# Kernel optimization log

Measured on AMD Instinct MI355X. Metric: run time of the kernel, lower is better.

The kernel has to match this reference:

```python
import jax, jax.numpy as jnp
import numpy as np

HEAD = 2

def conv1x1(w, x):
    # 1x1 Conv1d, bias=False: (O,C) x (B,C,N) -> (B,O,N)
    return jnp.einsum('oc,bcn->bon', w, x)

def setup_inputs() -> dict:
    key = jax.random.key(0)
    ks = jax.random.split(key, 14)
    B, Cin, N = 8, 64, 50000
    L, K = 256, 32
    tc, Cout = 128, 128
    def w(k, o, c):
        return jax.random.normal(k, (o, c), jnp.float32) * (1.0 / np.sqrt(c))
    return {
        'in_feature': jax.random.normal(ks[0], (B, Cin, N), jnp.float32),
        'in_tokens': jax.random.normal(ks[1], (B, tc, L), jnp.float32),
        'knn_idx': jax.random.randint(ks[2], (B, L, K), 0, N),
        # dynamic_f: conv1x1(Cin->tc), ReLU, conv1x1(tc->tc)  (norm = Identity)
        'w_dyn1': w(ks[3], tc, Cin),
        'w_dyn2': w(ks[4], tc, tc),
        # feature_block: conv1x1(Cin->Cout) since input_dims != output_dims
        'w_fb': w(ks[5], Cout, Cin),
        # Transformer (token self-attention + FFN)
        'w_k': w(ks[6], tc // 2, tc),
        'w_q': w(ks[7], tc // 2, tc),
        'w_v': w(ks[8], tc, tc),
        'w_ff1': w(ks[9], 2 * tc, tc),
        'w_ff2': w(ks[10], tc, 2 * tc),
        # Projector (tokens -> points cross-attention)
        'w_pv': w(ks[11], Cout, tc),
        'w_pk': w(ks[12], Cout, tc),
        'w_pq': w(ks[13], Cout, Cout),
    }

def reference(in_feature, in_tokens, w_dyn1, w_dyn2, w_fb,
              w_k, w_q, w_v, w_ff1, w_ff2, w_pv, w_pk, w_pq, knn_idx):
    B, C, N = in_feature.shape
    _, L, K = knn_idx.shape
    h = HEAD

    # ---- KNN gather + max-pool over K neighbors -> (B, C, L) ----
    idx = knn_idx.reshape(B, 1, L * K)                      # broadcast over C
    gathered = jnp.take_along_axis(in_feature, idx, axis=2).reshape(B, C, L, K)
    pooled = gathered.max(axis=3)                           # (B, C, L)

    # ---- dynamic_f: conv1x1 -> ReLU -> conv1x1 ----
    tokens = conv1x1(w_dyn2, jax.nn.relu(conv1x1(w_dyn1, pooled)))  # (B, tc, L)
    tokens = tokens + in_tokens

    # ---- Transformer over tokens ----
    tc = tokens.shape[1]
    k = conv1x1(w_k, tokens).reshape(B, h, -1, L)
    q = conv1x1(w_q, tokens).reshape(B, h, -1, L)
    v = conv1x1(w_v, tokens).reshape(B, h, -1, L)
    kq = jnp.einsum('bhdn,bhdm->bhnm', k, q)                # (B, h, L, L)
    attn = jax.nn.softmax(kq / np.sqrt(kq.shape[2]), axis=2)
    kqv = jnp.einsum('bhdn,bhnm->bhdm', v, attn).reshape(B, tc, L)
    t = tokens + kqv
    t = t + conv1x1(w_ff2, jax.nn.relu(conv1x1(w_ff1, t)))  # (B, tc, L)

    # ---- feature_block (input_dims != output_dims) ----
    x = conv1x1(w_fb, in_feature)                           # (B, Cout, N)
    d = x.shape[1]

    # ---- Projector: tokens -> per-point features ----
    pv = conv1x1(w_pv, t).reshape(B, h, -1, L)
    pk = conv1x1(w_pk, t).reshape(B, h, -1, L)
    pq = conv1x1(w_pq, x).reshape(B, h, -1, N)
    coef = jax.nn.softmax(
        jnp.einsum('bhdl,bhdn->bhln', pk, pq) / np.sqrt(d / h), axis=2)  # softmax over tokens
    out_feature = x + jnp.einsum('bhdl,bhln->bhdn', pv, coef).reshape(B, d, N)
    return out_feature, t
```

## Files before the change

### kernel.cpp

```cpp
#include <hip/hip_runtime.h>

#define B 8
#define CIN 64
#define NPT 50000
#define L 256
#define TC 128

typedef unsigned short ushort_t;
typedef __bf16 bf16x8 __attribute__((ext_vector_type(8)));
typedef float f32x4 __attribute__((ext_vector_type(4)));

__device__ __forceinline__ ushort_t f2b(float v) {
    union { float f; unsigned int u; } x; x.f = v;
    unsigned int r = x.u + 0x7FFFu + ((x.u >> 16) & 1u);
    return (ushort_t)(r >> 16);
}

__global__ void k_gather(const float* __restrict__ f, const int* __restrict__ knn,
                         float* __restrict__ pooled) {
    int id = blockIdx.x * 256 + threadIdx.x;
    int l = id & 255;
    int c = (id >> 8) & 63;
    int b = id >> 14;
    const int* kn = knn + (b * L + l) * 32;
    const float* fr = f + (b * CIN + c) * NPT;
    float m = -1e30f;
    #pragma unroll 8
    for (int k = 0; k < 32; k++) m = fmaxf(m, fr[kn[k]]);
    pooled[(b * CIN + c) * L + l] = m;
}

template <int O, int C, bool RELU>
__global__ void k_conv(const float* __restrict__ in, const float* __restrict__ w,
                       const float* __restrict__ res, float* __restrict__ out,
                       float* __restrict__ out2, ushort_t* __restrict__ outb) {
    int id = blockIdx.x * 256 + threadIdx.x;
    int l = id & 255;
    int o = (id >> 8) % O;
    int b = id / (O * 256);
    const float* ir = in + b * C * L + l;
    const float* wr = w + o * C;
    float acc = 0.f;
    #pragma unroll 8
    for (int c = 0; c < C; c++) acc += wr[c] * ir[c * L];
    if (RELU) acc = fmaxf(acc, 0.f);
    if (res) acc += res[id];
    if (out)  out[id] = acc;
    if (out2) out2[id] = acc;
    if (outb) outb[id] = f2b(acc);
}

__global__ void k_attn(const float* __restrict__ kmat, const float* __restrict__ qmat,
                       float* __restrict__ attn) {
    int blk = blockIdx.x;
    int m = blk & 255;
    int h = (blk >> 8) & 1;
    int b = blk >> 9;
    int n = threadIdx.x;
    const float* kr = kmat + (b * 64 + h * 32) * L + n;
    const float* qr = qmat + (b * 64 + h * 32) * L + m;
    float s = 0.f;
    #pragma unroll
    for (int d = 0; d < 32; d++) s += kr[d * L] * qr[d * L];
    s *= (1.f / 16.f);
    __shared__ float sm[256];
    sm[n] = s;
    __syncthreads();
    for (int st = 128; st > 0; st >>= 1) { if (n < st) sm[n] = fmaxf(sm[n], sm[n + st]); __syncthreads(); }
    float mx = sm[0];
    __syncthreads();
    float p = __expf(s - mx);
    sm[n] = p;
    __syncthreads();
    for (int st = 128; st > 0; st >>= 1) { if (n < st) sm[n] += sm[n + st]; __syncthreads(); }
    float Z = sm[0];
    attn[((b * 2 + h) * L + n) * L + m] = p / Z;
}

__global__ void k_kqv(const float* __restrict__ vmat, const float* __restrict__ attn,
                      const float* __restrict__ tokens, float* __restrict__ t1) {
    int id = blockIdx.x * 256 + threadIdx.x;
    int m = id & 255;
    int ch = (id >> 8) & 127;
    int b = id >> 15;
    int h = ch >> 6;
    const float* vr = vmat + (b * TC + ch) * L;
    const float* ar = attn + ((b * 2 + h) * L) * L + m;
    float acc = 0.f;
    #pragma unroll 8
    for (int n = 0; n < L; n++) acc += vr[n] * ar[n * L];
    t1[id] = tokens[id] + acc;
}

__global__ void k_pkq(const float* __restrict__ pk, const float* __restrict__ wpq,
                      ushort_t* __restrict__ pkqo) {
    int id = blockIdx.x * 256 + threadIdx.x;
    int e = id & 127;
    int l = (id >> 7) & 255;
    int h = (id >> 15) & 1;
    int b = id >> 16;
    const float* pkr = pk + (b * TC + h * 64) * L + l;
    const float* wr = wpq + (h * 64) * TC + e;
    float acc = 0.f;
    #pragma unroll 8
    for (int d = 0; d < 64; d++) acc += pkr[d * L] * wr[d * TC];
    pkqo[id] = f2b(acc * 0.125f);
}

__global__ void k_cvt_w(const float* __restrict__ w, ushort_t* __restrict__ o, int n) {
    int i = blockIdx.x * 256 + threadIdx.x;
    if (i < n) o[i] = f2b(w[i]);
}

__global__ __launch_bounds__(256) void k_proj(const float* __restrict__ f,
                                              const ushort_t* __restrict__ wfb16,
                                              const ushort_t* __restrict__ pkq16,
                                              const ushort_t* __restrict__ pv16,
                                              float* __restrict__ out, int N) {
    const int b = blockIdx.y;
    const int n0 = blockIdx.x * 64;
    const int tid = threadIdx.x;
    const int w = tid >> 6;
    const int lane = tid & 63;
    const int g = lane >> 4, cc = lane & 15;
    const int p = w * 16 + cc;

    __shared__ __align__(16) ushort_t Pl[4][4096];
    __shared__ __align__(16) ushort_t xt[64 * 128];
    ushort_t* ft = &Pl[0][0];

    #pragma unroll
    for (int i = 0; i < 16; i++) {
        int lin = tid + i * 256;
        int c = lin >> 6, pp = lin & 63;
        int n = n0 + pp;
        float v = (n < N) ? f[((size_t)b * CIN + c) * N + n] : 0.f;
        int idx = pp * 64 + ((((c >> 3) ^ (pp & 7)) << 3)) + (c & 7);
        ft[idx] = f2b(v);
    }
    __syncthreads();

    f32x4 xacc[8];
    #pragma unroll
    for (int et = 0; et < 8; et++) xacc[et] = (f32x4){0.f, 0.f, 0.f, 0.f};
    #pragma unroll
    for (int kk = 0; kk < 2; kk++) {
        bf16x8 fb = *(const bf16x8*)&ft[p * 64 + (((kk * 4 + g) ^ (cc & 7)) << 3)];
        #pragma unroll
        for (int et = 0; et < 8; et++) {
            bf16x8 a = *(const bf16x8*)&wfb16[(et * 16 + cc) * 64 + kk * 32 + g * 8];
            xacc[et] = __builtin_amdgcn_mfma_f32_16x16x32_bf16(a, fb, xacc[et], 0, 0, 0);
        }
    }
    __syncthreads();

    #pragma unroll
    for (int et = 0; et < 8; et++) {
        ushort4 q;
        q.x = f2b(xacc[et][0]); q.y = f2b(xacc[et][1]);
        q.z = f2b(xacc[et][2]); q.w = f2b(xacc[et][3]);
        int idx = p * 128 + ((((et * 2 + (g >> 1)) ^ (cc & 7)) << 3)) + (g & 1) * 4;
        *(ushort4*)&xt[idx] = q;
    }

    const size_t bN = (size_t)b * 128;

    for (int h = 0; h < 2; h++) {
        const ushort_t* pkqh = pkq16 + ((size_t)(b * 2 + h)) * 256 * 128;
        f32x4 sacc[16];
        #pragma unroll
        for (int lt = 0; lt < 16; lt++) sacc[lt] = (f32x4){0.f, 0.f, 0.f, 0.f};
        bf16x8 xb[4];
        #pragma unroll
        for (int ks = 0; ks < 4; ks++)
            xb[ks] = *(const bf16x8*)&xt[p * 128 + (((ks * 4 + g) ^ (cc & 7)) << 3)];
        #pragma unroll
        for (int lt = 0; lt < 16; lt++) {
            const ushort_t* arow = pkqh + (lt * 16 + cc) * 128 + g * 8;
            #pragma unroll
            for (int ks = 0; ks < 4; ks++) {
                bf16x8 a = *(const bf16x8*)&arow[ks * 32];
                sacc[lt] = __builtin_amdgcn_mfma_f32_16x16x32_bf16(a, xb[ks], sacc[lt], 0, 0, 0);
            }
        }

        float m = -1e30f;
        #pragma unroll
        for (int lt = 0; lt < 16; lt++) {
            m = fmaxf(m, fmaxf(fmaxf(sacc[lt][0], sacc[lt][1]), fmaxf(sacc[lt][2], sacc[lt][3])));
        }
        m = fmaxf(m, __shfl_xor(m, 16));
        m = fmaxf(m, __shfl_xor(m, 32));
        float z = 0.f;
        #pragma unroll
        for (int lt = 0; lt < 16; lt++) {
            float e0 = __expf(sacc[lt][0] - m), e1 = __expf(sacc[lt][1] - m);
            float e2 = __expf(sacc[lt][2] - m), e3 = __expf(sacc[lt][3] - m);
            z += (e0 + e1) + (e2 + e3);
            ushort4 q;
            q.x = f2b(e0); q.y = f2b(e1); q.z = f2b(e2); q.w = f2b(e3);
            int idx = cc * 256 + ((((lt * 2 + (g >> 1)) ^ (cc & 7)) << 3)) + (g & 1) * 4;
            *(ushort4*)&Pl[w][idx] = q;
        }
        z += __shfl_xor(z, 16);
        z += __shfl_xor(z, 32);

        f32x4 oacc[4];
        #pragma unroll
        for (int dt = 0; dt < 4; dt++) oacc[dt] = (f32x4){0.f, 0.f, 0.f, 0.f};
        const ushort_t* pvh = pv16 + (bN + h * 64) * 256;
        #pragma unroll
        for (int ks2 = 0; ks2 < 8; ks2++) {
            bf16x8 pb = *(const bf16x8*)&Pl[w][cc * 256 + (((ks2 * 4 + g) ^ (cc & 7)) << 3)];
            #pragma unroll
            for (int dt = 0; dt < 4; dt++) {
                bf16x8 a = *(const bf16x8*)&pvh[(dt * 16 + cc) * 256 + ks2 * 32 + g * 8];
                oacc[dt] = __builtin_amdgcn_mfma_f32_16x16x32_bf16(a, pb, oacc[dt], 0, 0, 0);
            }
        }

        float inv = 1.f / z;
        int n = n0 + p;
        if (n < N) {
            #pragma unroll
            for (int dt = 0; dt < 4; dt++) {
                #pragma unroll
                for (int r = 0; r < 4; r++) {
                    int d = h * 64 + dt * 16 + g * 4 + r;
                    out[(bN + d) * N + n] = xacc[h * 4 + dt][r] + oacc[dt][r] * inv;
                }
            }
        }
    }
}

extern "C" void kernel_launch(void* const* d_in, const int* in_sizes, int n_in,
                              void* d_out, int out_size, void* d_ws, size_t ws_size,
                              hipStream_t stream) {
    const float* f        = (const float*)d_in[0];
    const float* in_tok   = (const float*)d_in[1];
    const int*   knn      = (const int*)d_in[2];
    const float* w_dyn1   = (const float*)d_in[3];
    const float* w_dyn2   = (const float*)d_in[4];
    const float* w_fb     = (const float*)d_in[5];
    const float* w_k      = (const float*)d_in[6];
    const float* w_q      = (const float*)d_in[7];
    const float* w_v      = (const float*)d_in[8];
    const float* w_ff1    = (const float*)d_in[9];
    const float* w_ff2    = (const float*)d_in[10];
    const float* w_pv     = (const float*)d_in[11];
    const float* w_pk     = (const float*)d_in[12];
    const float* w_pq     = (const float*)d_in[13];

    float* out   = (float*)d_out;
    float* t_out = out + (size_t)B * 128 * NPT;

    float* ws     = (float*)d_ws;
    float* pooled = ws;
    float* tok1   = pooled + 131072;
    float* tokens = tok1 + 262144;
    float* kmat   = tokens + 262144;
    float* qmat   = kmat + 131072;
    float* vmat   = qmat + 131072;
    float* attn   = vmat + 262144;
    float* t1     = attn + 1048576;
    float* ff1    = t1 + 262144;
    float* tfin   = ff1 + 524288;
    float* pkb    = tfin + 262144;
    ushort_t* pkq16 = (ushort_t*)(pkb + 262144);
    ushort_t* pv16  = pkq16 + 524288;
    ushort_t* wfb16 = pv16 + 262144;

    k_cvt_w<<<32, 256, 0, stream>>>(w_fb, wfb16, 8192);
    k_gather<<<512, 256, 0, stream>>>(f, knn, pooled);
    k_conv<128, 64, true ><<<B * 128, 256, 0, stream>>>(pooled, w_dyn1, nullptr, tok1, nullptr, nullptr);
    k_conv<128, 128, false><<<B * 128, 256, 0, stream>>>(tok1, w_dyn2, in_tok, tokens, nullptr, nullptr);
    k_conv<64, 128, false><<<B * 64, 256, 0, stream>>>(tokens, w_k, nullptr, kmat, nullptr, nullptr);
    k_conv<64, 128, false><<<B * 64, 256, 0, stream>>>(tokens, w_q, nullptr, qmat, nullptr, nullptr);
    k_conv<128, 128, false><<<B * 128, 256, 0, stream>>>(tokens, w_v, nullptr, vmat, nullptr, nullptr);
    k_attn<<<B * 2 * 256, 256, 0, stream>>>(kmat, qmat, attn);
    k_kqv<<<B * 128, 256, 0, stream>>>(vmat, attn, tokens, t1);
    k_conv<256, 128, true ><<<B * 256, 256, 0, stream>>>(t1, w_ff1, nullptr, ff1, nullptr, nullptr);
    k_conv<128, 256, false><<<B * 128, 256, 0, stream>>>(ff1, w_ff2, t1, tfin, t_out, nullptr);
    k_conv<128, 128, false><<<B * 128, 256, 0, stream>>>(tfin, w_pv, nullptr, nullptr, nullptr, pv16);
    k_conv<128, 128, false><<<B * 128, 256, 0, stream>>>(tfin, w_pk, nullptr, pkb, nullptr, nullptr);
    k_pkq<<<2048, 256, 0, stream>>>(pkb, w_pq, pkq16);

    dim3 g((NPT + 63) / 64, B);
    k_proj<<<g, 256, 0, stream>>>(f, wfb16, pkq16, pv16, out, NPT);
}
```

Before: 1.033 ms.

## Stage projector pk/q and pv weights through double-buffered LDS via async global loads

Instead of each wave reading the pkq and pv weight tiles straight from global memory inside the MFMA loops, the projector kernel now copies 64-row chunks into a double-buffered LDS staging area with global_load_lds. The load of the next chunk is issued while the current one is consumed, with a block barrier per chunk. The aim is to share weight loads across the four waves and hide global latency. In exchange it costs 32KB of extra LDS, which may reduce occupancy, and adds eight barriers per head. The removed barrier after the ft read also relies on the later barriers for correctness with Pl aliasing.

```diff
diff --git a/kernel.cpp b/kernel.cpp
--- a/kernel.cpp
+++ b/kernel.cpp
@@ -14,6 +14,13 @@
     union { float f; unsigned int u; } x; x.f = v;
     unsigned int r = x.u + 0x7FFFu + ((x.u >> 16) & 1u);
     return (ushort_t)(r >> 16);
+}
+
+__device__ __forceinline__ void gl_lds16(const ushort_t* g, ushort_t* l) {
+    __builtin_amdgcn_global_load_lds(
+        (const __attribute__((address_space(1))) unsigned int*)g,
+        (__attribute__((address_space(3))) unsigned int*)l,
+        16, 0, 0);
 }
 
 __global__ void k_gather(const float* __restrict__ f, const int* __restrict__ knn,
@@ -127,8 +134,35 @@
 
     __shared__ __align__(16) ushort_t Pl[4][4096];
     __shared__ __align__(16) ushort_t xt[64 * 128];
+    __shared__ __align__(16) ushort_t stg[2][8192];
     ushort_t* ft = &Pl[0][0];
 
+    const size_t bN = (size_t)b * 128;
+    const ushort_t* pkqb = pkq16 + (size_t)(b * 2) * 256 * 128;
+    const ushort_t* pvb  = pv16 + bN * 256;
+
+    auto STAGE_PKQ = [&](int h, int ch, int buf) {
+        const ushort_t* src = pkqb + (size_t)h * 256 * 128 + ch * 64 * 128;
+        #pragma unroll
+        for (int i = 0; i < 4; i++) {
+            int bo = (w * 4 + i) * 64 + lane;
+            int row = bo >> 4, cb = bo & 15;
+            gl_lds16(src + row * 128 + ((cb ^ (row & 7)) << 3),
+                     &stg[buf][(w * 4 + i) * 512]);
+        }
+    };
+    auto STAGE_PV = [&](int h, int ch, int buf) {
+        const ushort_t* src = pvb + (size_t)h * 64 * 256 + ch * 64;
+        #pragma unroll
+        for (int i = 0; i < 2; i++) {
+            int bo = (w * 2 + i) * 64 + lane;
+            int row = bo >> 3, cb = bo & 7;
+            gl_lds16(src + row * 256 + ((cb ^ (row & 7)) << 3),
+                     &stg[buf][(w * 2 + i) * 512]);
+        }
+    };
+
+    STAGE_PKQ(0, 0, 0);
     #pragma unroll
     for (int i = 0; i < 16; i++) {
         int lin = tid + i * 256;
@@ -152,8 +186,6 @@
             xacc[et] = __builtin_amdgcn_mfma_f32_16x16x32_bf16(a, fb, xacc[et], 0, 0, 0);
         }
     }
-    __syncthreads();
-
     #pragma unroll
     for (int et = 0; et < 8; et++) {
         ushort4 q;
@@ -162,33 +194,38 @@
         int idx = p * 128 + ((((et * 2 + (g >> 1)) ^ (cc & 7)) << 3)) + (g & 1) * 4;
         *(ushort4*)&xt[idx] = q;
     }
-
-    const size_t bN = (size_t)b * 128;
-
+    bf16x8 xb[4];
+    #pragma unroll
+    for (int ks = 0; ks < 4; ks++)
+        xb[ks] = *(const bf16x8*)&xt[p * 128 + (((ks * 4 + g) ^ (cc & 7)) << 3)];
+
+    int buf = 0;
+    #pragma unroll
     for (int h = 0; h < 2; h++) {
-        const ushort_t* pkqh = pkq16 + ((size_t)(b * 2 + h)) * 256 * 128;
         f32x4 sacc[16];
         #pragma unroll
         for (int lt = 0; lt < 16; lt++) sacc[lt] = (f32x4){0.f, 0.f, 0.f, 0.f};
-        bf16x8 xb[4];
-        #pragma unroll
-        for (int ks = 0; ks < 4; ks++)
-            xb[ks] = *(const bf16x8*)&xt[p * 128 + (((ks * 4 + g) ^ (cc & 7)) << 3)];
-        #pragma unroll
-        for (int lt = 0; lt < 16; lt++) {
-            const ushort_t* arow = pkqh + (lt * 16 + cc) * 128 + g * 8;
+        #pragma unroll
+        for (int ch = 0; ch < 4; ch++) {
+            if (ch < 3) STAGE_PKQ(h, ch + 1, buf ^ 1);
+            else        STAGE_PV(h, 0, buf ^ 1);
             #pragma unroll
-            for (int ks = 0; ks < 4; ks++) {
-                bf16x8 a = *(const bf16x8*)&arow[ks * 32];
-                sacc[lt] = __builtin_amdgcn_mfma_f32_16x16x32_bf16(a, xb[ks], sacc[lt], 0, 0, 0);
+            for (int lt = 0; lt < 4; lt++) {
+                const int row = lt * 16 + cc;
+                #pragma unroll
+                for (int ks = 0; ks < 4; ks++) {
+                    bf16x8 a = *(const bf16x8*)&stg[buf][row * 128 + (((ks * 4 + g) ^ (cc & 7)) << 3)];
+                    sacc[ch * 4 + lt] = __builtin_amdgcn_mfma_f32_16x16x32_bf16(a, xb[ks], sacc[ch * 4 + lt], 0, 0, 0);
+                }
             }
+            __syncthreads();
+            buf ^= 1;
         }
 
         float m = -1e30f;
         #pragma unroll
-        for (int lt = 0; lt < 16; lt++) {
+        for (int lt = 0; lt < 16; lt++)
             m = fmaxf(m, fmaxf(fmaxf(sacc[lt][0], sacc[lt][1]), fmaxf(sacc[lt][2], sacc[lt][3])));
-        }
         m = fmaxf(m, __shfl_xor(m, 16));
         m = fmaxf(m, __shfl_xor(m, 32));
         float z = 0.f;
@@ -208,15 +245,22 @@
         f32x4 oacc[4];
         #pragma unroll
         for (int dt = 0; dt < 4; dt++) oacc[dt] = (f32x4){0.f, 0.f, 0.f, 0.f};
-        const ushort_t* pvh = pv16 + (bN + h * 64) * 256;
-        #pragma unroll
-        for (int ks2 = 0; ks2 < 8; ks2++) {
-            bf16x8 pb = *(const bf16x8*)&Pl[w][cc * 256 + (((ks2 * 4 + g) ^ (cc & 7)) << 3)];
+        #pragma unroll
+        for (int ch = 0; ch < 4; ch++) {
+            if (ch < 3)      STAGE_PV(h, ch + 1, buf ^ 1);
+            else if (h == 0) STAGE_PKQ(1, 0, buf ^ 1);
             #pragma unroll
             for (int dt = 0; dt < 4; dt++) {
-                bf16x8 a = *(const bf16x8*)&pvh[(dt * 16 + cc) * 256 + ks2 * 32 + g * 8];
-                oacc[dt] = __builtin_amdgcn_mfma_f32_16x16x32_bf16(a, pb, oacc[dt], 0, 0, 0);
+                const int row = dt * 16 + cc;
+                #pragma unroll
+                for (int ks2 = 0; ks2 < 2; ks2++) {
+                    bf16x8 a = *(const bf16x8*)&stg[buf][row * 64 + (((ks2 * 4 + g) ^ (cc & 7)) << 3)];
+                    bf16x8 pb = *(const bf16x8*)&Pl[w][cc * 256 + ((((ch * 2 + ks2) * 4 + g) ^ (cc & 7)) << 3)];
+                    oacc[dt] = __builtin_amdgcn_mfma_f32_16x16x32_bf16(a, pb, oacc[dt], 0, 0, 0);
+                }
             }
+            __syncthreads();
+            buf ^= 1;
         }
 
         float inv = 1.f / z;
```

Result: faster. 869.2 us (-15.8%).
